# Performance work log

Measured on AMD Instinct MI355X. Metric: run time of the kernel, lower is better.

The kernel has to match this reference:

```python
import jax, jax.numpy as jnp
import numpy as np

TEMP = 0.1
DX = 64  # feature dim of x; W1 rows [0:DX] multiply x, rows [DX:] multiply y


def setup_inputs() -> dict:
    key = jax.random.key(0)
    k1, k2, k3, k4 = jax.random.split(key, 4)
    n, d, hidden = 1024, 64, 256
    x = jax.random.normal(k1, (n, d), dtype=jnp.float32)
    y = jax.random.normal(k2, (n, d), dtype=jnp.float32)
    W1 = jax.random.normal(k3, (2 * d, hidden), dtype=jnp.float32) * (1.0 / np.sqrt(2 * d))
    b1 = jnp.zeros((hidden,), dtype=jnp.float32)
    w2 = jax.random.normal(k4, (hidden,), dtype=jnp.float32) * (1.0 / np.sqrt(hidden))
    b2 = jnp.zeros((), dtype=jnp.float32)
    return {"x": x, "y": y, "W1": W1, "b1": b1, "w2": w2, "b2": b2}


def reference(x, y, W1, b1, w2, b2):
    n = y.shape[0]
    W1x, W1y = W1[:DX], W1[DX:]
    xp = x @ W1x                      # [n, hidden], indexed by j (x_tile[i,j] = x[j])
    yp = y @ W1y                      # [n, hidden], indexed by i (y_tile[i,j] = y[i])
    # Positive pairs: scorer(cat(x_i, y_i))
    pos = (jax.nn.relu(xp + yp + b1) @ w2 + b2) / TEMP          # [n]
    h = jax.nn.relu(yp[:, None, :] + xp[None, :, :] + b1)        # [n, n, hidden]
    scores = (h @ w2 + b2) / TEMP                                 # [n, n]
    lse = jax.nn.logsumexp(scores, axis=1)                        # [n]
    lower_bound = pos.mean() - (lse.mean() - jnp.log(jnp.float32(n)))
    return -lower_bound
```

## Files before the change

### kernel.cpp

```cpp
#include <hip/hip_runtime.h>
#include <math.h>

#define NN 1024
#define DD 64
#define HH 256
#define TEMP_INV 10.0f
#define KCH 64
#define LPAD 34


__global__ __launch_bounds__(256)
void k1_proj(const float* __restrict__ x, const float* __restrict__ y,
             const float* __restrict__ W1, const float* __restrict__ b1,
             float* __restrict__ xpbT, float* __restrict__ ypT)
{
    const int tid = threadIdx.x;
    const int i0 = blockIdx.x * 2;
    float ax0 = 0.f, ax1 = 0.f, ay0 = 0.f, ay1 = 0.f;
    #pragma unroll 8
    for (int kk = 0; kk < DD; ++kk) {
        const float wx = W1[kk * HH + tid];
        const float wy = W1[(DD + kk) * HH + tid];
        ax0 = fmaf(x[i0 * DD + kk],       wx, ax0);
        ax1 = fmaf(x[(i0 + 1) * DD + kk], wx, ax1);
        ay0 = fmaf(y[i0 * DD + kk],       wy, ay0);
        ay1 = fmaf(y[(i0 + 1) * DD + kk], wy, ay1);
    }
    const float b1t = b1[tid];
    *(float2*)&xpbT[tid * NN + i0] = make_float2(ax0 + b1t, ax1 + b1t);
    *(float2*)&ypT[tid * NN + i0]  = make_float2(ay0, ay1);
}

__global__ __launch_bounds__(256, 4)
void k2_scores(const float* __restrict__ xpbT, const float* __restrict__ ypT,
               const float* __restrict__ w2, const float* __restrict__ b2,
               float* __restrict__ pmax, float* __restrict__ psum,
               float* __restrict__ pos)
{
    __shared__ float ys[KCH][LPAD];
    __shared__ float xs[KCH][LPAD];
    const int tid = threadIdx.x;
    const int jc = blockIdx.x, ic = blockIdx.y;
    const int i0 = ic * 32, j0 = jc * 32;
    const int lr = tid >> 4;
    const int lc = tid & 15;

    float a00 = 0.f, a01 = 0.f, a10 = 0.f, a11 = 0.f;

    for (int k0 = 0; k0 < HH; k0 += KCH) {
        __syncthreads();
        {
            const int u    = tid & 127;
            const int row  = u >> 1;
            const int half = (u & 1) * 16;
            const float* src = (tid >> 7) ? xpbT : ypT;
            const int    bas = (tid >> 7) ? j0 : i0;
            float* dst = (tid >> 7) ? &xs[row][half] : &ys[row][half];
            const float4 v0 = *(const float4*)&src[(k0 + row) * NN + bas + half + 0];
            const float4 v1 = *(const float4*)&src[(k0 + row) * NN + bas + half + 4];
            const float4 v2 = *(const float4*)&src[(k0 + row) * NN + bas + half + 8];
            const float4 v3 = *(const float4*)&src[(k0 + row) * NN + bas + half + 12];
            *(float2*)&dst[0]  = make_float2(v0.x, v0.y);
            *(float2*)&dst[2]  = make_float2(v0.z, v0.w);
            *(float2*)&dst[4]  = make_float2(v1.x, v1.y);
            *(float2*)&dst[6]  = make_float2(v1.z, v1.w);
            *(float2*)&dst[8]  = make_float2(v2.x, v2.y);
            *(float2*)&dst[10] = make_float2(v2.z, v2.w);
            *(float2*)&dst[12] = make_float2(v3.x, v3.y);
            *(float2*)&dst[14] = make_float2(v3.z, v3.w);
        }
        __syncthreads();

        #pragma unroll 8
        for (int kk = 0; kk < KCH; ++kk) {
            const float w2k = w2[k0 + kk];
            const float2 yv = *(const float2*)&ys[kk][lr * 2];
            const float2 xv = *(const float2*)&xs[kk][lc * 2];
            a00 = fmaf(fmaxf(yv.x + xv.x, 0.f), w2k, a00);
            a01 = fmaf(fmaxf(yv.x + xv.y, 0.f), w2k, a01);
            a10 = fmaf(fmaxf(yv.y + xv.x, 0.f), w2k, a10);
            a11 = fmaf(fmaxf(yv.y + xv.y, 0.f), w2k, a11);
        }
    }

    const float bb = b2[0];
    const float s00 = (a00 + bb) * TEMP_INV;
    const float s01 = (a01 + bb) * TEMP_INV;
    const float s10 = (a10 + bb) * TEMP_INV;
    const float s11 = (a11 + bb) * TEMP_INV;

    if (ic == jc && lr == lc) {
        pos[i0 + lr * 2]     = s00;
        pos[i0 + lr * 2 + 1] = s11;
    }

    float m0 = fmaxf(s00, s01);
    float e0 = __expf(s00 - m0) + __expf(s01 - m0);
    float m1 = fmaxf(s10, s11);
    float e1 = __expf(s10 - m1) + __expf(s11 - m1);
    #pragma unroll
    for (int mk = 8; mk >= 1; mk >>= 1) {
        const float m0o = __shfl_xor(m0, mk), e0o = __shfl_xor(e0, mk);
        const float m1o = __shfl_xor(m1, mk), e1o = __shfl_xor(e1, mk);
        float mn = fmaxf(m0, m0o);
        e0 = e0 * __expf(m0 - mn) + e0o * __expf(m0o - mn); m0 = mn;
        mn = fmaxf(m1, m1o);
        e1 = e1 * __expf(m1 - mn) + e1o * __expf(m1o - mn); m1 = mn;
    }
    if (lc == 0) {
        const int r0 = i0 + lr * 2;
        pmax[jc * NN + r0]     = m0;
        psum[jc * NN + r0]     = e0;
        pmax[jc * NN + r0 + 1] = m1;
        psum[jc * NN + r0 + 1] = e1;
    }
}

__global__ __launch_bounds__(1024)
void k3_final(const float* __restrict__ pmax, const float* __restrict__ psum,
              const float* __restrict__ pos, float* __restrict__ out)
{
    __shared__ float2 red[1024];
    const int tid = threadIdx.x;
    float M = pmax[tid], E = psum[tid];
    #pragma unroll 8
    for (int jc = 1; jc < 32; ++jc) {
        const float Mo = pmax[jc * NN + tid];
        const float Eo = psum[jc * NN + tid];
        const float Mn = fmaxf(M, Mo);
        E = E * __expf(M - Mn) + Eo * __expf(Mo - Mn);
        M = Mn;
    }
    red[tid] = make_float2(M + logf(E), pos[tid]);
    __syncthreads();
    for (int s = 512; s > 0; s >>= 1) {
        if (tid < s) {
            const float2 o = red[tid + s];
            float2 m2 = red[tid];
            m2.x += o.x; m2.y += o.y;
            red[tid] = m2;
        }
        __syncthreads();
    }
    if (tid == 0)
        out[0] = red[0].x / (float)NN - logf((float)NN) - red[0].y / (float)NN;
}

extern "C" void kernel_launch(void* const* d_in, const int* in_sizes, int n_in,
                              void* d_out, int out_size, void* d_ws, size_t ws_size,
                              hipStream_t stream)
{
    const float* x  = (const float*)d_in[0];
    const float* y  = (const float*)d_in[1];
    const float* W1 = (const float*)d_in[2];
    const float* b1 = (const float*)d_in[3];
    const float* w2 = (const float*)d_in[4];
    const float* b2 = (const float*)d_in[5];
    float* out = (float*)d_out;

    float* ws   = (float*)d_ws;
    float* xpbT = ws;
    float* ypT  = xpbT + HH * NN;
    float* pmax = ypT + HH * NN;
    float* psum = pmax + 32 * NN;
    float* pos  = psum + 32 * NN;

    hipLaunchKernelGGL(k1_proj, dim3(NN / 2), dim3(256), 0, stream,
                       x, y, W1, b1, xpbT, ypT);
    hipLaunchKernelGGL(k2_scores, dim3(32, 32), dim3(256), 0, stream,
                       xpbT, ypT, w2, b2, pmax, psum, pos);
    hipLaunchKernelGGL(k3_final, dim3(1), dim3(1024), 0, stream,
                       pmax, psum, pos, out);
}
```

Baseline: 43.10 us.

## Enlarge score tiles to 64x64 with double-buffered LDS and cached w2

The pairwise score kernel now has each block of 512 threads compute a 64x64 tile, with each thread accumulating 4x2 outputs instead of 2x2. The projection chunks are double-buffered in shared memory so the next chunk's loads overlap compute, and w2 is staged in LDS. The larger tile gives more reuse per loaded element and halves the partial-reduction slices, which k3 must now merge (16 instead of 32). The cost is that only 256 blocks launch on a GPU with many CUs, which lowers parallelism, and the unpadded 64-wide LDS rows may cause bank conflicts.

```diff
diff --git a/kernel.cpp b/kernel.cpp
--- a/kernel.cpp
+++ b/kernel.cpp
@@ -6,7 +6,7 @@
 #define HH 256
 #define TEMP_INV 10.0f
 #define KCH 64
-#define LPAD 34
+#define NCH (HH / KCH)
 
 
 __global__ __launch_bounds__(256)
@@ -31,88 +31,104 @@
     *(float2*)&ypT[tid * NN + i0]  = make_float2(ay0, ay1);
 }
 
-__global__ __launch_bounds__(256, 4)
+__global__ __launch_bounds__(512)
 void k2_scores(const float* __restrict__ xpbT, const float* __restrict__ ypT,
                const float* __restrict__ w2, const float* __restrict__ b2,
                float* __restrict__ pmax, float* __restrict__ psum,
                float* __restrict__ pos)
 {
-    __shared__ float ys[KCH][LPAD];
-    __shared__ float xs[KCH][LPAD];
-    const int tid = threadIdx.x;
-    const int jc = blockIdx.x, ic = blockIdx.y;
-    const int i0 = ic * 32, j0 = jc * 32;
-    const int lr = tid >> 4;
-    const int lc = tid & 15;
+    __shared__ float ys[2][KCH][64];
+    __shared__ float xs[2][KCH][64];
+    __shared__ float w2s[HH];
+    const int t  = threadIdx.x;
+    const int bj = blockIdx.x, bi = blockIdx.y;
+    const int i0 = bi * 64, j0 = bj * 64;
+    const int rr = t >> 5;
+    const int cc = t & 31;
 
-    float a00 = 0.f, a01 = 0.f, a10 = 0.f, a11 = 0.f;
+    if (t < HH) w2s[t] = w2[t];
 
-    for (int k0 = 0; k0 < HH; k0 += KCH) {
-        __syncthreads();
-        {
-            const int u    = tid & 127;
-            const int row  = u >> 1;
-            const int half = (u & 1) * 16;
-            const float* src = (tid >> 7) ? xpbT : ypT;
-            const int    bas = (tid >> 7) ? j0 : i0;
-            float* dst = (tid >> 7) ? &xs[row][half] : &ys[row][half];
-            const float4 v0 = *(const float4*)&src[(k0 + row) * NN + bas + half + 0];
-            const float4 v1 = *(const float4*)&src[(k0 + row) * NN + bas + half + 4];
-            const float4 v2 = *(const float4*)&src[(k0 + row) * NN + bas + half + 8];
-            const float4 v3 = *(const float4*)&src[(k0 + row) * NN + bas + half + 12];
-            *(float2*)&dst[0]  = make_float2(v0.x, v0.y);
-            *(float2*)&dst[2]  = make_float2(v0.z, v0.w);
-            *(float2*)&dst[4]  = make_float2(v1.x, v1.y);
-            *(float2*)&dst[6]  = make_float2(v1.z, v1.w);
-            *(float2*)&dst[8]  = make_float2(v2.x, v2.y);
-            *(float2*)&dst[10] = make_float2(v2.z, v2.w);
-            *(float2*)&dst[12] = make_float2(v3.x, v3.y);
-            *(float2*)&dst[14] = make_float2(v3.z, v3.w);
-        }
-        __syncthreads();
+    #define STAGE(c, buf)                                                      \
+    {                                                                          \
+        const int k0s = (c) * KCH;                                             \
+        _Pragma("unroll")                                                      \
+        for (int h = 0; h < 2; ++h) {                                          \
+            const int f  = t + h * 512;                                        \
+            const int r  = f >> 4;                                             \
+            const int c4 = (f & 15) * 4;                                       \
+            *(float4*)&ys[buf][r][c4] =                                        \
+                *(const float4*)&ypT[(k0s + r) * NN + i0 + c4];                \
+            *(float4*)&xs[buf][r][c4] =                                        \
+                *(const float4*)&xpbT[(k0s + r) * NN + j0 + c4];               \
+        }                                                                      \
+    }
 
+    float a00=0.f,a01=0.f, a10=0.f,a11=0.f, a20=0.f,a21=0.f, a30=0.f,a31=0.f;
+
+    STAGE(0, 0);
+    __syncthreads();
+    for (int c = 0; c < NCH; ++c) {
+        if (c + 1 < NCH) STAGE(c + 1, (c + 1) & 1);
+        const int k0 = c * KCH;
+        const int cur = c & 1;
         #pragma unroll 8
         for (int kk = 0; kk < KCH; ++kk) {
-            const float w2k = w2[k0 + kk];
-            const float2 yv = *(const float2*)&ys[kk][lr * 2];
-            const float2 xv = *(const float2*)&xs[kk][lc * 2];
+            const float w2k = w2s[k0 + kk];
+            const float4 yv = *(const float4*)&ys[cur][kk][rr * 4];
+            const float2 xv = *(const float2*)&xs[cur][kk][cc * 2];
             a00 = fmaf(fmaxf(yv.x + xv.x, 0.f), w2k, a00);
             a01 = fmaf(fmaxf(yv.x + xv.y, 0.f), w2k, a01);
             a10 = fmaf(fmaxf(yv.y + xv.x, 0.f), w2k, a10);
             a11 = fmaf(fmaxf(yv.y + xv.y, 0.f), w2k, a11);
+            a20 = fmaf(fmaxf(yv.z + xv.x, 0.f), w2k, a20);
+            a21 = fmaf(fmaxf(yv.z + xv.y, 0.f), w2k, a21);
+            a30 = fmaf(fmaxf(yv.w + xv.x, 0.f), w2k, a30);
+            a31 = fmaf(fmaxf(yv.w + xv.y, 0.f), w2k, a31);
+        }
+        __syncthreads();
+    }
+    #undef STAGE
+
+    const float bb = b2[0];
+    float s[4][2];
+    s[0][0] = (a00 + bb) * TEMP_INV; s[0][1] = (a01 + bb) * TEMP_INV;
+    s[1][0] = (a10 + bb) * TEMP_INV; s[1][1] = (a11 + bb) * TEMP_INV;
+    s[2][0] = (a20 + bb) * TEMP_INV; s[2][1] = (a21 + bb) * TEMP_INV;
+    s[3][0] = (a30 + bb) * TEMP_INV; s[3][1] = (a31 + bb) * TEMP_INV;
+
+    if (bi == bj) {
+        #pragma unroll
+        for (int p = 0; p < 4; ++p)
+            #pragma unroll
+            for (int q = 0; q < 2; ++q)
+                if (rr * 4 + p == cc * 2 + q)
+                    pos[i0 + rr * 4 + p] = s[p][q];
+    }
+
+    float m[4], e[4];
+    #pragma unroll
+    for (int p = 0; p < 4; ++p) {
+        m[p] = fmaxf(s[p][0], s[p][1]);
+        e[p] = __expf(s[p][0] - m[p]) + __expf(s[p][1] - m[p]);
+    }
+    #pragma unroll
+    for (int mk = 16; mk >= 1; mk >>= 1) {
+        #pragma unroll
+        for (int p = 0; p < 4; ++p) {
+            const float mo = __shfl_xor(m[p], mk);
+            const float eo = __shfl_xor(e[p], mk);
+            const float mn = fmaxf(m[p], mo);
+            e[p] = e[p] * __expf(m[p] - mn) + eo * __expf(mo - mn);
+            m[p] = mn;
         }
     }
-
-    const float bb = b2[0];
-    const float s00 = (a00 + bb) * TEMP_INV;
-    const float s01 = (a01 + bb) * TEMP_INV;
-    const float s10 = (a10 + bb) * TEMP_INV;
-    const float s11 = (a11 + bb) * TEMP_INV;
-
-    if (ic == jc && lr == lc) {
-        pos[i0 + lr * 2]     = s00;
-        pos[i0 + lr * 2 + 1] = s11;
-    }
-
-    float m0 = fmaxf(s00, s01);
-    float e0 = __expf(s00 - m0) + __expf(s01 - m0);
-    float m1 = fmaxf(s10, s11);
-    float e1 = __expf(s10 - m1) + __expf(s11 - m1);
-    #pragma unroll
-    for (int mk = 8; mk >= 1; mk >>= 1) {
-        const float m0o = __shfl_xor(m0, mk), e0o = __shfl_xor(e0, mk);
-        const float m1o = __shfl_xor(m1, mk), e1o = __shfl_xor(e1, mk);
-        float mn = fmaxf(m0, m0o);
-        e0 = e0 * __expf(m0 - mn) + e0o * __expf(m0o - mn); m0 = mn;
-        mn = fmaxf(m1, m1o);
-        e1 = e1 * __expf(m1 - mn) + e1o * __expf(m1o - mn); m1 = mn;
-    }
-    if (lc == 0) {
-        const int r0 = i0 + lr * 2;
-        pmax[jc * NN + r0]     = m0;
-        psum[jc * NN + r0]     = e0;
-        pmax[jc * NN + r0 + 1] = m1;
-        psum[jc * NN + r0 + 1] = e1;
+    if (cc == 0) {
+        #pragma unroll
+        for (int p = 0; p < 4; ++p) {
+            const int row = i0 + rr * 4 + p;
+            pmax[bj * NN + row] = m[p];
+            psum[bj * NN + row] = e[p];
+        }
     }
 }
 
@@ -123,8 +139,8 @@
     __shared__ float2 red[1024];
     const int tid = threadIdx.x;
     float M = pmax[tid], E = psum[tid];
-    #pragma unroll 8
-    for (int jc = 1; jc < 32; ++jc) {
+    #pragma unroll
+    for (int jc = 1; jc < 16; ++jc) {
         const float Mo = pmax[jc * NN + tid];
         const float Eo = psum[jc * NN + tid];
         const float Mn = fmaxf(M, Mo);
@@ -162,12 +178,12 @@
     float* xpbT = ws;
     float* ypT  = xpbT + HH * NN;
     float* pmax = ypT + HH * NN;
-    float* psum = pmax + 32 * NN;
-    float* pos  = psum + 32 * NN;
+    float* psum = pmax + 16 * NN;
+    float* pos  = psum + 16 * NN;
 
     hipLaunchKernelGGL(k1_proj, dim3(NN / 2), dim3(256), 0, stream,
                        x, y, W1, b1, xpbT, ypT);
-    hipLaunchKernelGGL(k2_scores, dim3(32, 32), dim3(256), 0, stream,
+    hipLaunchKernelGGL(k2_scores, dim3(16, 16), dim3(512), 0, stream,
                        xpbT, ypT, w2, b2, pmax, psum, pos);
     hipLaunchKernelGGL(k3_final, dim3(1), dim3(1024), 0, stream,
                        pmax, psum, pos, out);
```

Result: faster. 41.26 us (-4.3%).
